# Optimization experiments

Hardware: AMD Instinct MI355X
Metric: run time of the kernel (lower is better)

## Reference

```python
import jax, jax.numpy as jnp
import numpy as np

B, I, H, T = 64, 256, 512, 512


def setup_inputs() -> dict:
    key = jax.random.key(0)
    ks = jax.random.split(key, 7)
    x = jax.random.normal(ks[0], (B, I, T), jnp.float32)
    # PyTorch nn.LSTM default init: uniform(-1/sqrt(H), 1/sqrt(H))
    k = 1.0 / np.sqrt(H)
    W_ih = jax.random.uniform(ks[1], (4 * H, I), jnp.float32, -k, k)
    W_hh = jax.random.uniform(ks[2], (4 * H, H), jnp.float32, -k, k)
    b_ih = jax.random.uniform(ks[3], (4 * H,), jnp.float32, -k, k)
    b_hh = jax.random.uniform(ks[4], (4 * H,), jnp.float32, -k, k)
    # init_hidden: xavier_normal_ on zeros(1, B, H) -> N(0, std^2), std = sqrt(2/(fan_in+fan_out))
    # for a (1, B, H) tensor: fan_in = B*H, fan_out = 1*H
    std_h = np.sqrt(2.0 / (B * H + H)).astype(np.float32)
    h0 = std_h * jax.random.normal(ks[5], (B, H), jnp.float32)
    c0 = std_h * jax.random.normal(ks[6], (B, H), jnp.float32)
    return {"x": x, "W_ih": W_ih, "W_hh": W_hh, "b_ih": b_ih, "b_hh": b_hh,
            "h0": h0, "c0": c0}


def _lstm_scan(x, W_ih, W_hh, b_ih, b_hh, h0, c0):
    # x: (B, I, T) -> xs: (T, B, I); precompute input projections for all steps
    xs = jnp.transpose(x, (2, 0, 1))
    gx = jnp.einsum('tbi,gi->tbg', xs, W_ih) + (b_ih + b_hh)  # (T, B, 4H)

    def step(carry, gxt):
        h, c = carry
        gates = gxt + h @ W_hh.T  # (B, 4H)
        i_g, f_g, g_g, o_g = jnp.split(gates, 4, axis=-1)  # PyTorch gate order i,f,g,o
        i_g = jax.nn.sigmoid(i_g)
        f_g = jax.nn.sigmoid(f_g)
        g_g = jnp.tanh(g_g)
        o_g = jax.nn.sigmoid(o_g)
        c_new = f_g * c + i_g * g_g
        h_new = o_g * jnp.tanh(c_new)
        return (h_new, c_new), h_new

    (_, _), hs = jax.lax.scan(step, (h0, c0), gx)  # hs: (T, B, H)
    encoded = jnp.transpose(hs, (1, 2, 0))  # (B, H, T)
    return hs[-1][None], encoded  # mirrors (_, input_encoded)


def reference(x, W_ih, W_hh, b_ih, b_hh, h0, c0):
    return _lstm_scan(x, W_ih, W_hh, b_ih, b_hh, h0, c0)
```

## Files before the change

### kernel.cpp

```cpp
#include <hip/hip_runtime.h>

constexpr int B_ = 64, I_ = 256, H_ = 512, T_ = 512;
constexpr int BH_ = B_ * H_;

constexpr size_t WS_XT_OFF = 524288;

typedef float f32x4 __attribute__((ext_vector_type(4)));
typedef _Float16 h2 __attribute__((ext_vector_type(2)));
typedef _Float16 h8v __attribute__((ext_vector_type(8)));
union H8 { h8v v; h2 p[4]; };

#if defined(__has_builtin)
#if __has_builtin(__builtin_amdgcn_fdot2)
#define HAVE_FDOT2 1
#endif
#endif

__device__ __forceinline__ float dot2(h2 a, h2 b, float c) {
#ifdef HAVE_FDOT2
    return __builtin_amdgcn_fdot2(a, b, c, false);
#else
    return c + (float)a[0] * (float)b[0] + (float)a[1] * (float)b[1];
#endif
}

__device__ __forceinline__ float sigm(float v) { return 1.0f / (1.0f + __expf(-v)); }
__device__ __forceinline__ float tanh_fast(float v) {
    float e = __expf(2.0f * v);
    return 1.0f - 2.0f / (e + 1.0f);
}

__global__ __launch_bounds__(256)
void transpose_x(const float* __restrict__ x, _Float16* __restrict__ xT)
{
    __shared__ float tile[32][33];
    const int b  = blockIdx.z;
    const int i0 = blockIdx.y << 5;
    const int t0 = blockIdx.x << 5;
    const int lt = threadIdx.x;
    const int li = threadIdx.y;
#pragma unroll
    for (int r = 0; r < 4; ++r) {
        int i = li + (r << 3);
        tile[i][lt] = x[((size_t)b * I_ + (i0 + i)) * T_ + (t0 + lt)];
    }
    __syncthreads();
#pragma unroll
    for (int r = 0; r < 4; ++r) {
        int tt = li + (r << 3);
        xT[((size_t)(t0 + tt) * B_ + b) * I_ + (i0 + lt)] = (_Float16)tile[lt][tt];
    }
}

__global__ __launch_bounds__(512, 1)
void lstm_fused(const float* __restrict__ x,
                const _Float16* __restrict__ xT,
                const float* __restrict__ Wih,
                const float* __restrict__ Whh,
                const float* __restrict__ bih,
                const float* __restrict__ bhh,
                const float* __restrict__ h0,
                const float* __restrict__ c0,
                float* __restrict__ out,
                float* __restrict__ hbuf)
{
    __shared__ __align__(16) char smem[47232];
    f32x4* redA  = (f32x4*)smem;
    h2*    actx2 = (h2*)(smem + 34048);
    h2*    acth2 = (h2*)(smem + 34048 + 4224);
    float* hsh   = (float*)(smem + 34048 + 4224 + 8448);

    const int tid  = threadIdx.x;
    const int wv   = tid >> 6;
    const int lane = tid & 63;
    const int jl   = lane & 15;
    const int slq  = lane >> 4;
    const int bg   = wv >> 2;
    const int sl16 = ((wv & 3) << 2) | slq;

    const int blk = blockIdx.x;
    const int bt  = blk >> 5;
    const int jt  = blk & 31;
    const int b0  = bt << 3;
    const int j0  = jt << 4;

    const int j = j0 + jl;
    h2 wx2[4][8];
    h2 wh2[4][16];
#pragma unroll
    for (int g = 0; g < 4; ++g) {
        const size_t row = (size_t)(g * H_ + j);
#pragma unroll
        for (int q = 0; q < 8; ++q) {
            wx2[g][q][0] = (_Float16)Wih[row * I_ + (sl16 << 4) + 2 * q];
            wx2[g][q][1] = (_Float16)Wih[row * I_ + (sl16 << 4) + 2 * q + 1];
        }
#pragma unroll
        for (int q = 0; q < 16; ++q) {
            wh2[g][q][0] = (_Float16)Whh[row * H_ + (sl16 << 5) + 2 * q];
            wh2[g][q][1] = (_Float16)Whh[row * H_ + (sl16 << 5) + 2 * q + 1];
        }
    }

    const int fb = b0 + (tid >> 4);
    const int fj = j0 + (tid & 15);
    float c = 0.f;
    f32x4 bias4 = {0.f, 0.f, 0.f, 0.f};
    if (tid < 128) {
        c = c0[(size_t)fb * H_ + fj];
#pragma unroll
        for (int g = 0; g < 4; ++g) bias4[g] = bih[g * H_ + fj] + bhh[g * H_ + fj];
    }

    float* enc = out + BH_;

    const int sb     = (bg << 2) + (lane >> 4);
    const int hb_off = ((wv & 3) << 7) + ((lane & 15) << 3);
    h2* hdst = acth2 + sb * 264 + (hb_off >> 1);

    uint2 xv;
    if (xT) xv = *(const uint2*)(xT + (size_t)b0 * I_ + tid * 4);

    for (int t = 0; t < T_; ++t) {
        if (xT) {
            *(uint2*)((char*)(actx2 + (size_t)(tid >> 6) * 132) + (size_t)(tid & 63) * 8) = xv;
        } else {
#pragma unroll
            for (int r = 0; r < 4; ++r) {
                int flat = tid + (r << 9), bb = flat >> 8, ii = flat & 255;
                ((_Float16*)(actx2 + (size_t)bb * 132))[ii] =
                    (_Float16)x[((size_t)(b0 + bb) * I_ + ii) * T_ + t];
            }
        }
        __syncthreads();

        f32x4 v0, v1;
        const float* hsrc = hbuf + (size_t)((t - 1) & 1) * BH_
                          + (size_t)(b0 + sb) * H_ + hb_off;
        if (t > 0) {
            asm volatile("global_load_dwordx4 %0, %2, off sc0 sc1\n\t"
                         "global_load_dwordx4 %1, %3, off sc0 sc1"
                         : "=&v"(v0), "=&v"(v1) : "v"(hsrc), "v"(hsrc + 4));
            __builtin_amdgcn_sched_barrier(0);
        }

        f32x4 r4[4];
#pragma unroll
        for (int i = 0; i < 4; ++i) {
            const int bq = (bg << 2) + i;
            H8 ax0, ax1;
            ax0.v = *(const h8v*)(actx2 + (size_t)bq * 132 + (sl16 << 3));
            ax1.v = *(const h8v*)(actx2 + (size_t)bq * 132 + (sl16 << 3) + 4);
            float s0 = 0.f, s1 = 0.f, s2 = 0.f, s3 = 0.f;
#pragma unroll
            for (int q = 0; q < 4; ++q) {
                s0 = dot2(ax0.p[q], wx2[0][q], s0);
                s1 = dot2(ax0.p[q], wx2[1][q], s1);
                s2 = dot2(ax0.p[q], wx2[2][q], s2);
                s3 = dot2(ax0.p[q], wx2[3][q], s3);
            }
#pragma unroll
            for (int q = 0; q < 4; ++q) {
                s0 = dot2(ax1.p[q], wx2[0][q + 4], s0);
                s1 = dot2(ax1.p[q], wx2[1][q + 4], s1);
                s2 = dot2(ax1.p[q], wx2[2][q + 4], s2);
                s3 = dot2(ax1.p[q], wx2[3][q + 4], s3);
            }
            r4[i] = (f32x4){s0, s1, s2, s3};
        }

        if (t > 0) {
            asm volatile("s_waitcnt vmcnt(0)" ::: "memory");
            __builtin_amdgcn_sched_barrier(0);
            const float Kc = 2.0f + 2.0f * (float)(((t - 1) >> 1) & 1);
            bool ok = true;
#pragma unroll
            for (int e = 0; e < 4; ++e) {
                ok = ok && (fabsf(v0[e] - Kc) < 0.75f);
                ok = ok && (fabsf(v1[e] - Kc) < 0.75f);
            }
            for (unsigned it = 0; !ok && it < 32768u; ++it) {
                __builtin_amdgcn_s_sleep(1);
                asm volatile("global_load_dwordx4 %0, %2, off sc0 sc1\n\t"
                             "global_load_dwordx4 %1, %3, off sc0 sc1\n\t"
                             "s_waitcnt vmcnt(0)"
                             : "=&v"(v0), "=&v"(v1) : "v"(hsrc), "v"(hsrc + 4) : "memory");
                ok = true;
#pragma unroll
                for (int e = 0; e < 4; ++e) {
                    ok = ok && (fabsf(v0[e] - Kc) < 0.75f);
                    ok = ok && (fabsf(v1[e] - Kc) < 0.75f);
                }
            }
            v0 = (v0 - Kc) * 2.0f;
            v1 = (v1 - Kc) * 2.0f;
        } else {
            const float* src = h0 + (size_t)(b0 + sb) * H_ + hb_off;
            v0 = *(const f32x4*)src;
            v1 = *(const f32x4*)(src + 4);
        }
        {
            H8 hv;
#pragma unroll
            for (int e = 0; e < 2; ++e) { hv.p[e][0]   = (_Float16)v0[2*e];
                                          hv.p[e][1]   = (_Float16)v0[2*e+1];
                                          hv.p[e+2][0] = (_Float16)v1[2*e];
                                          hv.p[e+2][1] = (_Float16)v1[2*e+1]; }
            *(h8v*)hdst = hv.v;
            asm volatile("s_waitcnt lgkmcnt(0)" ::: "memory");
            __builtin_amdgcn_sched_barrier(0);
        }

        if (xT && t + 1 < T_)
            xv = *(const uint2*)(xT + ((size_t)(t + 1) * B_ + b0) * I_ + tid * 4);

#pragma unroll
        for (int i = 0; i < 4; ++i) {
            const int bq = (bg << 2) + i;
            const h2* hrow = acth2 + (size_t)bq * 264 + (sl16 << 4);
            H8 a0, a1, a2, a3;
            a0.v = *(const h8v*)(hrow);
            a1.v = *(const h8v*)(hrow + 4);
            a2.v = *(const h8v*)(hrow + 8);
            a3.v = *(const h8v*)(hrow + 12);
            float s0 = r4[i][0], s1 = r4[i][1], s2 = r4[i][2], s3 = r4[i][3];
#pragma unroll
            for (int q = 0; q < 4; ++q) {
                s0 = dot2(a0.p[q], wh2[0][q], s0);
                s1 = dot2(a0.p[q], wh2[1][q], s1);
                s2 = dot2(a0.p[q], wh2[2][q], s2);
                s3 = dot2(a0.p[q], wh2[3][q], s3);
            }
#pragma unroll
            for (int q = 0; q < 4; ++q) {
                s0 = dot2(a1.p[q], wh2[0][q + 4], s0);
                s1 = dot2(a1.p[q], wh2[1][q + 4], s1);
                s2 = dot2(a1.p[q], wh2[2][q + 4], s2);
                s3 = dot2(a1.p[q], wh2[3][q + 4], s3);
            }
#pragma unroll
            for (int q = 0; q < 4; ++q) {
                s0 = dot2(a2.p[q], wh2[0][q + 8], s0);
                s1 = dot2(a2.p[q], wh2[1][q + 8], s1);
                s2 = dot2(a2.p[q], wh2[2][q + 8], s2);
                s3 = dot2(a2.p[q], wh2[3][q + 8], s3);
            }
#pragma unroll
            for (int q = 0; q < 4; ++q) {
                s0 = dot2(a3.p[q], wh2[0][q + 12], s0);
                s1 = dot2(a3.p[q], wh2[1][q + 12], s1);
                s2 = dot2(a3.p[q], wh2[2][q + 12], s2);
                s3 = dot2(a3.p[q], wh2[3][q + 12], s3);
            }
            r4[i] = (f32x4){s0, s1, s2, s3};
        }

#pragma unroll
        for (int i = 0; i < 4; ++i)
            redA[sl16 * 133 + (((bg << 2) + i) << 4) + jl] = r4[i];
        __syncthreads();

        if (tid < 128) {
            f32x4 G = bias4;
#pragma unroll
            for (int s = 0; s < 16; ++s) G += redA[s * 133 + tid];
            float ig = sigm(G[0]), fg = sigm(G[1]);
            float gg = tanh_fast(G[2]);
            float og = sigm(G[3]);
            c = fg * c + ig * gg;
            float hv = og * tanh_fast(c);
            hsh[tid] = hv;
            enc[((size_t)fb * H_ + fj) * T_ + t] = hv;
            if (t == T_ - 1) {
                out[(size_t)fb * H_ + fj] = hv;
            } else {
                asm volatile("s_waitcnt lgkmcnt(0)" ::: "memory");
                __builtin_amdgcn_sched_barrier(0);
                if (lane < 16) {
                    const float Kp = 2.0f + 2.0f * (float)((t >> 1) & 1);
                    f32x4 v = *(const f32x4*)(&hsh[(wv << 6) + ((lane >> 2) << 4) + ((lane & 3) << 2)]);
                    v = v * 0.5f + Kp;
                    float* dst = hbuf + (size_t)(t & 1) * BH_
                               + (size_t)(b0 + (wv << 2) + (lane >> 2)) * H_
                               + j0 + ((lane & 3) << 2);
                    asm volatile("global_store_dwordx4 %0, %1, off sc0 sc1"
                                 :: "v"(dst), "v"(v) : "memory");
                }
            }
        }
    }
}

extern "C" void kernel_launch(void* const* d_in, const int* in_sizes, int n_in,
                              void* d_out, int out_size, void* d_ws, size_t ws_size,
                              hipStream_t stream)
{
    (void)in_sizes; (void)n_in; (void)out_size;
    const float* x   = (const float*)d_in[0];
    const float* Wih = (const float*)d_in[1];
    const float* Whh = (const float*)d_in[2];
    const float* bih = (const float*)d_in[3];
    const float* bhh = (const float*)d_in[4];
    const float* h0  = (const float*)d_in[5];
    const float* c0  = (const float*)d_in[6];
    float* out  = (float*)d_out;
    float* hbuf = (float*)d_ws;

    const size_t xt_bytes = (size_t)T_ * B_ * I_ * sizeof(_Float16);
    _Float16* xT = nullptr;
    if (ws_size >= WS_XT_OFF + xt_bytes)
        xT = (_Float16*)((char*)d_ws + WS_XT_OFF);

    hipMemsetAsync(d_ws, 0, 2 * BH_ * sizeof(float), stream);
    if (xT)
        transpose_x<<<dim3(T_ / 32, I_ / 32, B_), dim3(32, 8), 0, stream>>>(x, xT);

    void* args[] = { (void*)&x, (void*)&xT, (void*)&Wih, (void*)&Whh, (void*)&bih,
                     (void*)&bhh, (void*)&h0, (void*)&c0, (void*)&out, (void*)&hbuf };
    hipLaunchCooperativeKernel((void*)lstm_fused, dim3(256), dim3(512), args, 0, stream);
}
```

Measured before the change: 1.652 ms.

## Split LSTM work into smaller 256-thread blocks with two blocks per CU

Adds a variant of the persistent cooperative LSTM kernel that uses 512 blocks of 256 threads, each handling 8 hidden units instead of 16, with two blocks resident per CU. Each thread now covers 16 input and 32 hidden elements, loading four dwordx4 hidden vectors per step, and the shared-memory reduction spans 16 slices. The launcher queries occupancy and falls back to the original 512-thread kernel if two blocks cannot fit. The transposed-x path becomes mandatory and the unchecked workspace assumption is dropped. More blocks means more polling traffic and more cross-block synchronisation per step, in exchange for spreading the work over more CUs.

```diff
diff --git a/kernel.cpp b/kernel.cpp
--- a/kernel.cpp
+++ b/kernel.cpp
@@ -52,9 +52,8 @@
     }
 }
 
-__global__ __launch_bounds__(512, 1)
-void lstm_fused(const float* __restrict__ x,
-                const _Float16* __restrict__ xT,
+__global__ __launch_bounds__(256, 2)
+void lstm_small(const _Float16* __restrict__ xT,
                 const float* __restrict__ Wih,
                 const float* __restrict__ Whh,
                 const float* __restrict__ bih,
@@ -64,6 +63,244 @@
                 float* __restrict__ out,
                 float* __restrict__ hbuf)
 {
+    __shared__ __align__(16) char smem[30592];
+    f32x4* redA  = (f32x4*)smem;
+    h2*    actx2 = (h2*)(smem + 17664);
+    h2*    acth2 = (h2*)(smem + 17664 + 4224);
+    float* hsh   = (float*)(smem + 17664 + 4224 + 8448);
+
+    const int tid  = threadIdx.x;
+    const int wv   = tid >> 6;
+    const int lane = tid & 63;
+    const int jl   = lane & 7;
+    const int slq  = lane >> 3;
+    const int bg   = wv >> 1;
+    const int sl16 = ((wv & 1) << 3) | slq;
+
+    const int blk = blockIdx.x;
+    const int bt  = blk >> 6;
+    const int jt8 = blk & 63;
+    const int b0  = bt << 3;
+    const int j0  = jt8 << 3;
+
+    const int j = j0 + jl;
+    h2 wx2[4][8];
+    h2 wh2[4][16];
+#pragma unroll
+    for (int g = 0; g < 4; ++g) {
+        const size_t row = (size_t)(g * H_ + j);
+#pragma unroll
+        for (int q = 0; q < 8; ++q) {
+            wx2[g][q][0] = (_Float16)Wih[row * I_ + (sl16 << 4) + 2 * q];
+            wx2[g][q][1] = (_Float16)Wih[row * I_ + (sl16 << 4) + 2 * q + 1];
+        }
+#pragma unroll
+        for (int q = 0; q < 16; ++q) {
+            wh2[g][q][0] = (_Float16)Whh[row * H_ + (sl16 << 5) + 2 * q];
+            wh2[g][q][1] = (_Float16)Whh[row * H_ + (sl16 << 5) + 2 * q + 1];
+        }
+    }
+
+    const int fb = b0 + (tid >> 3);
+    const int fj = j0 + (tid & 7);
+    float c = 0.f;
+    f32x4 bias4 = {0.f, 0.f, 0.f, 0.f};
+    if (tid < 64) {
+        c = c0[(size_t)fb * H_ + fj];
+#pragma unroll
+        for (int g = 0; g < 4; ++g) bias4[g] = bih[g * H_ + fj] + bhh[g * H_ + fj];
+    }
+
+    float* enc = out + BH_;
+
+    const int sb     = (bg << 2) + (lane >> 4);
+    const int hb_off = ((wv & 1) << 8) + ((lane & 15) << 4);
+    h2* hdst = acth2 + sb * 264 + (hb_off >> 1);
+
+    float4 xv = *(const float4*)(xT + (size_t)b0 * I_ + tid * 8);
+
+    for (int t = 0; t < T_; ++t) {
+        *(float4*)((char*)(actx2 + (size_t)(tid >> 5) * 132) + (size_t)(tid & 31) * 16) = xv;
+        __syncthreads();
+
+        f32x4 v0, v1, v2, v3;
+        const float* hsrc = hbuf + (size_t)((t - 1) & 1) * BH_
+                          + (size_t)(b0 + sb) * H_ + hb_off;
+        if (t > 0) {
+            asm volatile("global_load_dwordx4 %0, %4, off sc0 sc1\n\t"
+                         "global_load_dwordx4 %1, %5, off sc0 sc1\n\t"
+                         "global_load_dwordx4 %2, %6, off sc0 sc1\n\t"
+                         "global_load_dwordx4 %3, %7, off sc0 sc1"
+                         : "=&v"(v0), "=&v"(v1), "=&v"(v2), "=&v"(v3)
+                         : "v"(hsrc), "v"(hsrc + 4), "v"(hsrc + 8), "v"(hsrc + 12));
+            __builtin_amdgcn_sched_barrier(0);
+        }
+
+        f32x4 r4[4];
+#pragma unroll
+        for (int i = 0; i < 4; ++i) {
+            const int bq = (bg << 2) + i;
+            H8 ax0, ax1;
+            ax0.v = *(const h8v*)(actx2 + (size_t)bq * 132 + (sl16 << 3));
+            ax1.v = *(const h8v*)(actx2 + (size_t)bq * 132 + (sl16 << 3) + 4);
+            float s0 = 0.f, s1 = 0.f, s2 = 0.f, s3 = 0.f;
+#pragma unroll
+            for (int q = 0; q < 4; ++q) {
+                s0 = dot2(ax0.p[q], wx2[0][q], s0);
+                s1 = dot2(ax0.p[q], wx2[1][q], s1);
+                s2 = dot2(ax0.p[q], wx2[2][q], s2);
+                s3 = dot2(ax0.p[q], wx2[3][q], s3);
+            }
+#pragma unroll
+            for (int q = 0; q < 4; ++q) {
+                s0 = dot2(ax1.p[q], wx2[0][q + 4], s0);
+                s1 = dot2(ax1.p[q], wx2[1][q + 4], s1);
+                s2 = dot2(ax1.p[q], wx2[2][q + 4], s2);
+                s3 = dot2(ax1.p[q], wx2[3][q + 4], s3);
+            }
+            r4[i] = (f32x4){s0, s1, s2, s3};
+        }
+
+        if (t > 0) {
+            asm volatile("s_waitcnt vmcnt(0)" ::: "memory");
+            __builtin_amdgcn_sched_barrier(0);
+            const float Kc = 2.0f + 2.0f * (float)(((t - 1) >> 1) & 1);
+            bool ok = true;
+#pragma unroll
+            for (int e = 0; e < 4; ++e) {
+                ok = ok && (fabsf(v0[e] - Kc) < 0.75f) && (fabsf(v1[e] - Kc) < 0.75f);
+                ok = ok && (fabsf(v2[e] - Kc) < 0.75f) && (fabsf(v3[e] - Kc) < 0.75f);
+            }
+            for (unsigned it = 0; !ok && it < 32768u; ++it) {
+                __builtin_amdgcn_s_sleep(1);
+                asm volatile("global_load_dwordx4 %0, %4, off sc0 sc1\n\t"
+                             "global_load_dwordx4 %1, %5, off sc0 sc1\n\t"
+                             "global_load_dwordx4 %2, %6, off sc0 sc1\n\t"
+                             "global_load_dwordx4 %3, %7, off sc0 sc1\n\t"
+                             "s_waitcnt vmcnt(0)"
+                             : "=&v"(v0), "=&v"(v1), "=&v"(v2), "=&v"(v3)
+                             : "v"(hsrc), "v"(hsrc + 4), "v"(hsrc + 8), "v"(hsrc + 12)
+                             : "memory");
+                ok = true;
+#pragma unroll
+                for (int e = 0; e < 4; ++e) {
+                    ok = ok && (fabsf(v0[e] - Kc) < 0.75f) && (fabsf(v1[e] - Kc) < 0.75f);
+                    ok = ok && (fabsf(v2[e] - Kc) < 0.75f) && (fabsf(v3[e] - Kc) < 0.75f);
+                }
+            }
+            v0 = (v0 - Kc) * 2.0f;  v1 = (v1 - Kc) * 2.0f;
+            v2 = (v2 - Kc) * 2.0f;  v3 = (v3 - Kc) * 2.0f;
+        } else {
+            const float* src = h0 + (size_t)(b0 + sb) * H_ + hb_off;
+            v0 = *(const f32x4*)src;       v1 = *(const f32x4*)(src + 4);
+            v2 = *(const f32x4*)(src + 8); v3 = *(const f32x4*)(src + 12);
+        }
+        {
+            H8 ha, hb;
+#pragma unroll
+            for (int e = 0; e < 2; ++e) {
+                ha.p[e][0]   = (_Float16)v0[2*e]; ha.p[e][1]   = (_Float16)v0[2*e+1];
+                ha.p[e+2][0] = (_Float16)v1[2*e]; ha.p[e+2][1] = (_Float16)v1[2*e+1];
+                hb.p[e][0]   = (_Float16)v2[2*e]; hb.p[e][1]   = (_Float16)v2[2*e+1];
+                hb.p[e+2][0] = (_Float16)v3[2*e]; hb.p[e+2][1] = (_Float16)v3[2*e+1];
+            }
+            *(h8v*)hdst = ha.v;
+            *(h8v*)(hdst + 4) = hb.v;
+            asm volatile("s_waitcnt lgkmcnt(0)" ::: "memory");
+            __builtin_amdgcn_sched_barrier(0);
+        }
+
+        if (t + 1 < T_)
+            xv = *(const float4*)(xT + ((size_t)(t + 1) * B_ + b0) * I_ + tid * 8);
+
+#pragma unroll
+        for (int i = 0; i < 4; ++i) {
+            const int bq = (bg << 2) + i;
+            const h2* hrow = acth2 + (size_t)bq * 264 + (sl16 << 4);
+            H8 a0, a1, a2, a3;
+            a0.v = *(const h8v*)(hrow);
+            a1.v = *(const h8v*)(hrow + 4);
+            a2.v = *(const h8v*)(hrow + 8);
+            a3.v = *(const h8v*)(hrow + 12);
+            float s0 = r4[i][0], s1 = r4[i][1], s2 = r4[i][2], s3 = r4[i][3];
+#pragma unroll
+            for (int q = 0; q < 4; ++q) {
+                s0 = dot2(a0.p[q], wh2[0][q], s0);
+                s1 = dot2(a0.p[q], wh2[1][q], s1);
+                s2 = dot2(a0.p[q], wh2[2][q], s2);
+                s3 = dot2(a0.p[q], wh2[3][q], s3);
+            }
+#pragma unroll
+            for (int q = 0; q < 4; ++q) {
+                s0 = dot2(a1.p[q], wh2[0][q + 4], s0);
+                s1 = dot2(a1.p[q], wh2[1][q + 4], s1);
+                s2 = dot2(a1.p[q], wh2[2][q + 4], s2);
+                s3 = dot2(a1.p[q], wh2[3][q + 4], s3);
+            }
+#pragma unroll
+            for (int q = 0; q < 4; ++q) {
+                s0 = dot2(a2.p[q], wh2[0][q + 8], s0);
+                s1 = dot2(a2.p[q], wh2[1][q + 8], s1);
+                s2 = dot2(a2.p[q], wh2[2][q + 8], s2);
+                s3 = dot2(a2.p[q], wh2[3][q + 8], s3);
+            }
+#pragma unroll
+            for (int q = 0; q < 4; ++q) {
+                s0 = dot2(a3.p[q], wh2[0][q + 12], s0);
+                s1 = dot2(a3.p[q], wh2[1][q + 12], s1);
+                s2 = dot2(a3.p[q], wh2[2][q + 12], s2);
+                s3 = dot2(a3.p[q], wh2[3][q + 12], s3);
+            }
+            r4[i] = (f32x4){s0, s1, s2, s3};
+        }
+
+#pragma unroll
+        for (int i = 0; i < 4; ++i)
+            redA[sl16 * 69 + ((((bg << 2) + i)) << 3) + jl] = r4[i];
+        __syncthreads();
+
+        if (tid < 64) {
+            f32x4 G = bias4;
+#pragma unroll
+            for (int s = 0; s < 16; ++s) G += redA[s * 69 + tid];
+            float ig = sigm(G[0]), fg = sigm(G[1]);
+            float gg = tanh_fast(G[2]);
+            float og = sigm(G[3]);
+            c = fg * c + ig * gg;
+            float hv = og * tanh_fast(c);
+            hsh[tid] = hv;
+            if (t == T_ - 1) {
+                enc[((size_t)fb * H_ + fj) * T_ + t] = hv;
+                out[(size_t)fb * H_ + fj] = hv;
+            } else {
+                asm volatile("s_waitcnt lgkmcnt(0)" ::: "memory");
+                __builtin_amdgcn_sched_barrier(0);
+                if (lane < 16) {
+                    const float Kp = 2.0f + 2.0f * (float)((t >> 1) & 1);
+                    f32x4 v = *(const f32x4*)(&hsh[lane << 2]);
+                    v = v * 0.5f + Kp;
+                    float* dst = hbuf + (size_t)(t & 1) * BH_
+                               + (size_t)(b0 + (lane >> 1)) * H_ + j0 + ((lane & 1) << 2);
+                    asm volatile("global_store_dwordx4 %0, %1, off sc0 sc1"
+                                 :: "v"(dst), "v"(v) : "memory");
+                }
+                enc[((size_t)fb * H_ + fj) * T_ + t] = hv;
+            }
+        }
+    }
+}
+
+__global__ __launch_bounds__(512, 1)
+void lstm_big(const _Float16* __restrict__ xT,
+              const float* __restrict__ Wih,
+              const float* __restrict__ Whh,
+              const float* __restrict__ bih,
+              const float* __restrict__ bhh,
+              const float* __restrict__ h0,
+              const float* __restrict__ c0,
+              float* __restrict__ out,
+              float* __restrict__ hbuf)
+{
     __shared__ __align__(16) char smem[47232];
     f32x4* redA  = (f32x4*)smem;
     h2*    actx2 = (h2*)(smem + 34048);
@@ -113,25 +350,14 @@
     }
 
     float* enc = out + BH_;
-
     const int sb     = (bg << 2) + (lane >> 4);
     const int hb_off = ((wv & 3) << 7) + ((lane & 15) << 3);
     h2* hdst = acth2 + sb * 264 + (hb_off >> 1);
 
-    uint2 xv;
-    if (xT) xv = *(const uint2*)(xT + (size_t)b0 * I_ + tid * 4);
+    uint2 xv = *(const uint2*)(xT + (size_t)b0 * I_ + tid * 4);
 
     for (int t = 0; t < T_; ++t) {
-        if (xT) {
-            *(uint2*)((char*)(actx2 + (size_t)(tid >> 6) * 132) + (size_t)(tid & 63) * 8) = xv;
-        } else {
-#pragma unroll
-            for (int r = 0; r < 4; ++r) {
-                int flat = tid + (r << 9), bb = flat >> 8, ii = flat & 255;
-                ((_Float16*)(actx2 + (size_t)bb * 132))[ii] =
-                    (_Float16)x[((size_t)(b0 + bb) * I_ + ii) * T_ + t];
-            }
-        }
+        *(uint2*)((char*)(actx2 + (size_t)(tid >> 6) * 132) + (size_t)(tid & 63) * 8) = xv;
         __syncthreads();
 
         f32x4 v0, v1;
@@ -211,7 +437,7 @@
             __builtin_amdgcn_sched_barrier(0);
         }
 
-        if (xT && t + 1 < T_)
+        if (t + 1 < T_)
             xv = *(const uint2*)(xT + ((size_t)(t + 1) * B_ + b0) * I_ + tid * 4);
 
 #pragma unroll
@@ -305,17 +531,19 @@
     const float* c0  = (const float*)d_in[6];
     float* out  = (float*)d_out;
     float* hbuf = (float*)d_ws;
-
-    const size_t xt_bytes = (size_t)T_ * B_ * I_ * sizeof(_Float16);
-    _Float16* xT = nullptr;
-    if (ws_size >= WS_XT_OFF + xt_bytes)
-        xT = (_Float16*)((char*)d_ws + WS_XT_OFF);
+    _Float16* xT = (_Float16*)((char*)d_ws + WS_XT_OFF);
 
     hipMemsetAsync(d_ws, 0, 2 * BH_ * sizeof(float), stream);
-    if (xT)
-        transpose_x<<<dim3(T_ / 32, I_ / 32, B_), dim3(32, 8), 0, stream>>>(x, xT);
-
-    void* args[] = { (void*)&x, (void*)&xT, (void*)&Wih, (void*)&Whh, (void*)&bih,
+    transpose_x<<<dim3(T_ / 32, I_ / 32, B_), dim3(32, 8), 0, stream>>>(x, xT);
+
+    void* args[] = { (void*)&xT, (void*)&Wih, (void*)&Whh, (void*)&bih,
                      (void*)&bhh, (void*)&h0, (void*)&c0, (void*)&out, (void*)&hbuf };
-    hipLaunchCooperativeKernel((void*)lstm_fused, dim3(256), dim3(512), args, 0, stream);
+
+    int occ = 0;
+    hipError_t qe = hipOccupancyMaxActiveBlocksPerMultiprocessor(&occ, lstm_small, 256, 0);
+    if (qe == hipSuccess && occ >= 2) {
+        hipLaunchCooperativeKernel((void*)lstm_small, dim3(512), dim3(256), args, 0, stream);
+    } else {
+        hipLaunchCooperativeKernel((void*)lstm_big, dim3(256), dim3(512), args, 0, stream);
+    }
 }
```

Measured after the change: 1.652 ms. No clear change (+0.0%).

## Double-buffer x tile in LDS and drop per-step barrier before x use

Applied to the files above, without the earlier changes.

Double-buffers the per-step fp16 input slice in shared memory, writing step t+1's slice during step t and prefetching step t+2 from global. This removes one __syncthreads per timestep, since the existing end-of-step barrier now covers the x buffer. It also skips the sleep on the first two polling iterations of the cross-block h exchange, and moves the encoded-output store after the h publish so the critical-path store goes out first. The fallback path that read x directly is removed, so the code now assumes the workspace is large enough for the transposed copy.

```diff
diff --git a/kernel.cpp b/kernel.cpp
--- a/kernel.cpp
+++ b/kernel.cpp
@@ -53,8 +53,7 @@
 }
 
 __global__ __launch_bounds__(512, 1)
-void lstm_fused(const float* __restrict__ x,
-                const _Float16* __restrict__ xT,
+void lstm_fused(const _Float16* __restrict__ xT,
                 const float* __restrict__ Wih,
                 const float* __restrict__ Whh,
                 const float* __restrict__ bih,
@@ -64,11 +63,11 @@
                 float* __restrict__ out,
                 float* __restrict__ hbuf)
 {
-    __shared__ __align__(16) char smem[47232];
+    __shared__ __align__(16) char smem[51456];
     f32x4* redA  = (f32x4*)smem;
     h2*    actx2 = (h2*)(smem + 34048);
-    h2*    acth2 = (h2*)(smem + 34048 + 4224);
-    float* hsh   = (float*)(smem + 34048 + 4224 + 8448);
+    h2*    acth2 = (h2*)(smem + 34048 + 8448);
+    float* hsh   = (float*)(smem + 34048 + 8448 + 8448);
 
     const int tid  = threadIdx.x;
     const int wv   = tid >> 6;
@@ -119,20 +118,15 @@
     h2* hdst = acth2 + sb * 264 + (hb_off >> 1);
 
     uint2 xv;
-    if (xT) xv = *(const uint2*)(xT + (size_t)b0 * I_ + tid * 4);
+    {
+        uint2 x0 = *(const uint2*)(xT + (size_t)b0 * I_ + tid * 4);
+        *(uint2*)((char*)(actx2 + (size_t)(tid >> 6) * 132) + (size_t)(tid & 63) * 8) = x0;
+        xv = *(const uint2*)(xT + ((size_t)B_ + (size_t)b0) * I_ + tid * 4);
+    }
+    __syncthreads();
 
     for (int t = 0; t < T_; ++t) {
-        if (xT) {
-            *(uint2*)((char*)(actx2 + (size_t)(tid >> 6) * 132) + (size_t)(tid & 63) * 8) = xv;
-        } else {
-#pragma unroll
-            for (int r = 0; r < 4; ++r) {
-                int flat = tid + (r << 9), bb = flat >> 8, ii = flat & 255;
-                ((_Float16*)(actx2 + (size_t)bb * 132))[ii] =
-                    (_Float16)x[((size_t)(b0 + bb) * I_ + ii) * T_ + t];
-            }
-        }
-        __syncthreads();
+        const h2* actxb = actx2 + (size_t)(t & 1) * 1056;
 
         f32x4 v0, v1;
         const float* hsrc = hbuf + (size_t)((t - 1) & 1) * BH_
@@ -149,8 +143,8 @@
         for (int i = 0; i < 4; ++i) {
             const int bq = (bg << 2) + i;
             H8 ax0, ax1;
-            ax0.v = *(const h8v*)(actx2 + (size_t)bq * 132 + (sl16 << 3));
-            ax1.v = *(const h8v*)(actx2 + (size_t)bq * 132 + (sl16 << 3) + 4);
+            ax0.v = *(const h8v*)(actxb + (size_t)bq * 132 + (sl16 << 3));
+            ax1.v = *(const h8v*)(actxb + (size_t)bq * 132 + (sl16 << 3) + 4);
             float s0 = 0.f, s1 = 0.f, s2 = 0.f, s3 = 0.f;
 #pragma unroll
             for (int q = 0; q < 4; ++q) {
@@ -180,7 +174,7 @@
                 ok = ok && (fabsf(v1[e] - Kc) < 0.75f);
             }
             for (unsigned it = 0; !ok && it < 32768u; ++it) {
-                __builtin_amdgcn_s_sleep(1);
+                if (it >= 2) __builtin_amdgcn_s_sleep(1);
                 asm volatile("global_load_dwordx4 %0, %2, off sc0 sc1\n\t"
                              "global_load_dwordx4 %1, %3, off sc0 sc1\n\t"
                              "s_waitcnt vmcnt(0)"
@@ -210,9 +204,6 @@
             asm volatile("s_waitcnt lgkmcnt(0)" ::: "memory");
             __builtin_amdgcn_sched_barrier(0);
         }
-
-        if (xT && t + 1 < T_)
-            xv = *(const uint2*)(xT + ((size_t)(t + 1) * B_ + b0) * I_ + tid * 4);
 
 #pragma unroll
         for (int i = 0; i < 4; ++i) {
@@ -255,6 +246,13 @@
             r4[i] = (f32x4){s0, s1, s2, s3};
         }
 
+        if (t + 1 < T_) {
+            *(uint2*)((char*)(actx2 + (size_t)((t + 1) & 1) * 1056
+                              + (size_t)(tid >> 6) * 132) + (size_t)(tid & 63) * 8) = xv;
+            if (t + 2 < T_)
+                xv = *(const uint2*)(xT + ((size_t)(t + 2) * B_ + b0) * I_ + tid * 4);
+        }
+
 #pragma unroll
         for (int i = 0; i < 4; ++i)
             redA[sl16 * 133 + (((bg << 2) + i) << 4) + jl] = r4[i];
@@ -270,8 +268,8 @@
             c = fg * c + ig * gg;
             float hv = og * tanh_fast(c);
             hsh[tid] = hv;
-            enc[((size_t)fb * H_ + fj) * T_ + t] = hv;
             if (t == T_ - 1) {
+                enc[((size_t)fb * H_ + fj) * T_ + t] = hv;
                 out[(size_t)fb * H_ + fj] = hv;
             } else {
                 asm volatile("s_waitcnt lgkmcnt(0)" ::: "memory");
@@ -286,6 +284,7 @@
                     asm volatile("global_store_dwordx4 %0, %1, off sc0 sc1"
                                  :: "v"(dst), "v"(v) : "memory");
                 }
+                enc[((size_t)fb * H_ + fj) * T_ + t] = hv;
             }
         }
     }
@@ -295,7 +294,7 @@
                               void* d_out, int out_size, void* d_ws, size_t ws_size,
                               hipStream_t stream)
 {
-    (void)in_sizes; (void)n_in; (void)out_size;
+    (void)in_sizes; (void)n_in; (void)out_size; (void)ws_size;
     const float* x   = (const float*)d_in[0];
     const float* Wih = (const float*)d_in[1];
     const float* Whh = (const float*)d_in[2];
@@ -305,17 +304,12 @@
     const float* c0  = (const float*)d_in[6];
     float* out  = (float*)d_out;
     float* hbuf = (float*)d_ws;
-
-    const size_t xt_bytes = (size_t)T_ * B_ * I_ * sizeof(_Float16);
-    _Float16* xT = nullptr;
-    if (ws_size >= WS_XT_OFF + xt_bytes)
-        xT = (_Float16*)((char*)d_ws + WS_XT_OFF);
+    _Float16* xT = (_Float16*)((char*)d_ws + WS_XT_OFF);
 
     hipMemsetAsync(d_ws, 0, 2 * BH_ * sizeof(float), stream);
-    if (xT)
-        transpose_x<<<dim3(T_ / 32, I_ / 32, B_), dim3(32, 8), 0, stream>>>(x, xT);
-
-    void* args[] = { (void*)&x, (void*)&xT, (void*)&Wih, (void*)&Whh, (void*)&bih,
+    transpose_x<<<dim3(T_ / 32, I_ / 32, B_), dim3(32, 8), 0, stream>>>(x, xT);
+
+    void* args[] = { (void*)&xT, (void*)&Wih, (void*)&Whh, (void*)&bih,
                      (void*)&bhh, (void*)&h0, (void*)&c0, (void*)&out, (void*)&hbuf };
     hipLaunchCooperativeKernel((void*)lstm_fused, dim3(256), dim3(512), args, 0, stream);
 }
```

Result: slower. 2.154 ms (+30.4%).
